# Kernel tuning notes

Measured on AMD Instinct MI355X. Metric: run time of the kernel, lower is better.

Reference implementation:

```python
import jax, jax.numpy as jnp
import numpy as np

B, C, E = 2, 1024, 1024
H = 16            # n_heads as declared (used as per-group feature dim due to module's reshape)
HD = E // H       # 64 — the axis actually batched over in attention


def setup_inputs() -> dict:
    key = jax.random.key(0)
    ks = jax.random.split(key, 5)
    scale = 0.02
    return {
        "x": jax.random.normal(ks[0], (B, C, E), dtype=jnp.float32),
        "W_q": jax.random.normal(ks[1], (E, E), dtype=jnp.float32) * scale,
        "W_k": jax.random.normal(ks[2], (E, E), dtype=jnp.float32) * scale,
        "W_v": jax.random.normal(ks[3], (E, E), dtype=jnp.float32) * scale,
        "W_o": jax.random.normal(ks[4], (E, E), dtype=jnp.float32) * scale,
    }


def reference(x, W_q, W_k, W_v, W_o):
    # nn.Linear: y = x @ W.T  (bias=False)
    def proj_split(W):
        y = jnp.einsum('bce,de->bcd', x, W)              # [B,C,E]
        # view(B, C, HD, H).transpose(1,2) -> [B, HD, C, H]  (faithful to source layout)
        return y.reshape(B, C, HD, H).transpose(0, 2, 1, 3)

    Q = proj_split(W_q)
    K = proj_split(W_k)
    V = proj_split(W_v)

    scale = 1.0 / jnp.sqrt(jnp.asarray(H, dtype=x.dtype))  # sqrt of last dim (= n_heads here)
    scores = jnp.einsum('bdqh,bdkh->bdqk', Q, K) * scale    # [B, HD, C, C]
    weights = jax.nn.softmax(scores, axis=-1)
    out = jnp.einsum('bdqk,bdkh->bdqh', weights, V)         # [B, HD, C, H]
    out = out.transpose(0, 2, 1, 3).reshape(B, C, E)        # [B, C, E]
    out = jnp.einsum('bce,de->bcd', out, W_o)
    return out  # dropout p=0.0 / eval mode: identity
```

## Files before the change

kernel.cpp:

```cpp
#include <hip/hip_runtime.h>
#include <stdint.h>
#include <math.h>


typedef __bf16   bf16x8 __attribute__((ext_vector_type(8)));
typedef float    f32x4  __attribute__((ext_vector_type(4)));

__device__ __forceinline__ unsigned short f2bf(float f) {
    unsigned int u = __float_as_uint(f);
    u += 0x7FFFu + ((u >> 16) & 1u);
    return (unsigned short)(u >> 16);
}
__device__ __forceinline__ float bflo(unsigned int u) { return __uint_as_float(u << 16); }
__device__ __forceinline__ float bfhi(unsigned int u) { return __uint_as_float(u & 0xFFFF0000u); }

__device__ __forceinline__ unsigned int pkbf(float lo, float hi) {
    const unsigned int ulo = __float_as_uint(lo) + 0x8000u;
    const unsigned int uhi = __float_as_uint(hi) + 0x8000u;
    return __builtin_amdgcn_perm(uhi, ulo, 0x07060302u);
}

__global__ __launch_bounds__(256) void cast_to_bf16(
    const float* __restrict__ x,
    const float* __restrict__ w0, const float* __restrict__ w1,
    const float* __restrict__ w2, const float* __restrict__ w3,
    unsigned short* __restrict__ xb,
    unsigned short* __restrict__ b0, unsigned short* __restrict__ b1,
    unsigned short* __restrict__ b2, unsigned short* __restrict__ b3)
{
    const int z = blockIdx.y;
    const float* src;
    unsigned short* dst;
    size_t off = 0;
    float sc = 1.f;
    if (z < 2)       { src = x;  dst = xb; off = (size_t)z << 20; }
    else if (z == 2) { src = w0; dst = b0; sc = 0.36067376022224085f; }
    else if (z == 3) { src = w1; dst = b1; }
    else if (z == 4) { src = w2; dst = b2; }
    else             { src = w3; dst = b3; }
    const size_t i = off + ((size_t)blockIdx.x * 256 + threadIdx.x) * 4;
    const float4 v = *(const float4*)(src + i);
    *(ushort4*)(dst + i) = make_ushort4(f2bf(v.x * sc), f2bf(v.y * sc),
                                        f2bf(v.z * sc), f2bf(v.w * sc));
}

__global__ __launch_bounds__(256) void gemm_bt_mfma(
    const unsigned short* __restrict__ A,
    const unsigned short* __restrict__ B0, const unsigned short* __restrict__ B1,
    const unsigned short* __restrict__ B2,
    void* __restrict__ C0, void* __restrict__ C1, void* __restrict__ C2,
    int M, int N, int K, int bf16out)
{
    const unsigned short* Bm = (blockIdx.z == 0) ? B0 : (blockIdx.z == 1) ? B1 : B2;
    void* Cm                 = (blockIdx.z == 0) ? C0 : (blockIdx.z == 1) ? C1 : C2;

    __shared__ __align__(16) unsigned short As[64 * 32];
    __shared__ __align__(16) unsigned short Bs[128 * 32];

    const int t    = threadIdx.x;
    const int lane = t & 63;
    const int w    = t >> 6;
    const int m0   = blockIdx.y * 64;
    const int n0   = blockIdx.x * 128;
    const int wm   = (w & 1) * 32;
    const int wn   = (w >> 1) * 64;

    const int r0 = t >> 2;
    const int c0 = (t & 3) * 8;
    const unsigned short* Apa = A  + (size_t)(m0 + r0) * K + c0;
    const unsigned short* Bpa = Bm + (size_t)(n0 + r0) * K + c0;
    const unsigned short* Bpb = Bm + (size_t)(n0 + r0 + 64) * K + c0;

    f32x4 acc[2][4];
#pragma unroll
    for (int i = 0; i < 2; ++i)
#pragma unroll
        for (int j = 0; j < 4; ++j) acc[i][j] = (f32x4){0.f, 0.f, 0.f, 0.f};

    const int fm = lane & 15;
    const int kg = lane >> 4;

    uint4 ra0 = *(const uint4*)(Apa);
    uint4 rb0 = *(const uint4*)(Bpa);
    uint4 rb1 = *(const uint4*)(Bpb);

    for (int k0 = 0; k0 < K; k0 += 32) {
        if (k0) __syncthreads();
        *(uint4*)&As[8 * t]        = ra0;
        *(uint4*)&Bs[8 * t]        = rb0;
        *(uint4*)&Bs[8 * t + 2048] = rb1;
        __syncthreads();

        if (k0 + 32 < K) {
            ra0 = *(const uint4*)(Apa + k0 + 32);
            rb0 = *(const uint4*)(Bpa + k0 + 32);
            rb1 = *(const uint4*)(Bpb + k0 + 32);
        }

        bf16x8 af[2], bfr[4];
#pragma unroll
        for (int im = 0; im < 2; ++im)
            af[im] = *(const bf16x8*)&As[(wm + im * 16 + fm) * 32 + kg * 8];
#pragma unroll
        for (int in = 0; in < 4; ++in)
            bfr[in] = *(const bf16x8*)&Bs[(wn + in * 16 + fm) * 32 + kg * 8];
#pragma unroll
        for (int im = 0; im < 2; ++im)
#pragma unroll
            for (int in = 0; in < 4; ++in)
                acc[im][in] = __builtin_amdgcn_mfma_f32_16x16x32_bf16(
                    af[im], bfr[in], acc[im][in], 0, 0, 0);
    }

#pragma unroll
    for (int im = 0; im < 2; ++im) {
#pragma unroll
        for (int in = 0; in < 4; ++in) {
            const int row = m0 + wm + im * 16 + kg * 4;
            const int col = n0 + wn + in * 16 + fm;
            if (bf16out) {
                unsigned short* cp = (unsigned short*)Cm;
#pragma unroll
                for (int r = 0; r < 4; ++r)
                    cp[(size_t)(row + r) * N + col] = f2bf(acc[im][in][r]);
            } else {
                float* cp = (float*)Cm;
#pragma unroll
                for (int r = 0; r < 4; ++r)
                    cp[(size_t)(row + r) * N + col] = acc[im][in][r];
            }
        }
    }
}

#define KSTR2 40
#define VSTR2 72
#define PSTR  80

__global__ __launch_bounds__(256) void attn_mfma(
    const unsigned short* __restrict__ Qb, const unsigned short* __restrict__ Kb,
    const unsigned short* __restrict__ Vb, unsigned short* __restrict__ Ob)
{
    __shared__ __align__(16) unsigned short Ks[64 * KSTR2];
    __shared__ __align__(16) unsigned short VsT[16 * VSTR2];
    __shared__ __align__(16) unsigned short Ps[128 * PSTR];
    __shared__ __align__(16) float Lsh[128];

    const int t    = threadIdx.x;
    const int lane = t & 63;
    const int wq   = t >> 6;
    const int fm   = lane & 15;
    const int kg   = lane >> 4;
    const int bh   = blockIdx.y;
    const size_t base = ((size_t)(bh >> 6) * 1024) * 1024 + (size_t)(bh & 63) * 16;
    const int q0 = blockIdx.x * 128;

    if (t < 128) {
        const int row = t >> 1, seg = t & 1;
        *(uint4*)&Ks[row * KSTR2 + 16 + seg * 8] = make_uint4(0, 0, 0, 0);
    }

    union { uint4 u; bf16x8 h; } zz; zz.u = make_uint4(0, 0, 0, 0);
    bf16x8 aq[2];
#pragma unroll
    for (int m = 0; m < 2; ++m) {
        if (kg < 2)
            aq[m] = *(const bf16x8*)(Qb + base +
                     (size_t)(q0 + wq * 32 + m * 16 + fm) * 1024 + kg * 8);
        else
            aq[m] = zz.h;
    }

    f32x4 oacc[2];
    float lp[2];
#pragma unroll
    for (int m = 0; m < 2; ++m) {
        oacc[m] = (f32x4){0.f, 0.f, 0.f, 0.f};
        lp[m] = 0.f;
    }

    for (int kt = 0; kt < 1024; kt += 64) {
        __syncthreads();
        if (t < 128) {
            const int row = t >> 1, seg = t & 1;
            *(uint4*)&Ks[row * KSTR2 + seg * 8] =
                *(const uint4*)(Kb + base + (size_t)(kt + row) * 1024 + seg * 8);
        } else {
            const int idx = t - 128;
            const int key = idx >> 1, half = idx & 1;
            uint4 v = *(const uint4*)(Vb + base + (size_t)(kt + key) * 1024 + half * 8);
            const unsigned short* pv = (const unsigned short*)&v;
#pragma unroll
            for (int d = 0; d < 8; ++d)
                VsT[(half * 8 + d) * VSTR2 + key] = pv[d];
        }
        __syncthreads();

        bf16x8 bk[4];
#pragma unroll
        for (int kn = 0; kn < 4; ++kn)
            bk[kn] = *(const bf16x8*)&Ks[(kn * 16 + fm) * KSTR2 + kg * 8];

#pragma unroll
        for (int kn = 0; kn < 4; ++kn) {
            f32x4 sm[2];
#pragma unroll
            for (int m = 0; m < 2; ++m)
                sm[m] = __builtin_amdgcn_mfma_f32_16x16x32_bf16(
                    bk[kn], aq[m], (f32x4){0.f, 0.f, 0.f, 0.f}, 0, 0, 0);
#pragma unroll
            for (int m = 0; m < 2; ++m) {
                const float p0 = __builtin_amdgcn_exp2f(sm[m][0]);
                const float p1 = __builtin_amdgcn_exp2f(sm[m][1]);
                const float p2 = __builtin_amdgcn_exp2f(sm[m][2]);
                const float p3 = __builtin_amdgcn_exp2f(sm[m][3]);
                lp[m] += (p0 + p1) + (p2 + p3);
                *(uint2*)&Ps[(wq * 32 + m * 16 + fm) * PSTR + kn * 16 + kg * 4] =
                    make_uint2(pkbf(p0, p1), pkbf(p2, p3));
            }
        }

        bf16x8 bv0 = *(const bf16x8*)&VsT[fm * VSTR2 + kg * 8];
        bf16x8 bv1 = *(const bf16x8*)&VsT[fm * VSTR2 + 32 + kg * 8];
#pragma unroll
        for (int m = 0; m < 2; ++m) {
            const int prow = wq * 32 + m * 16 + fm;
            bf16x8 ap0 = *(const bf16x8*)&Ps[prow * PSTR + kg * 8];
            bf16x8 ap1 = *(const bf16x8*)&Ps[prow * PSTR + 32 + kg * 8];
            oacc[m] = __builtin_amdgcn_mfma_f32_16x16x32_bf16(ap0, bv0, oacc[m], 0, 0, 0);
            oacc[m] = __builtin_amdgcn_mfma_f32_16x16x32_bf16(ap1, bv1, oacc[m], 0, 0, 0);
        }
    }

#pragma unroll
    for (int m = 0; m < 2; ++m) {
        float v = lp[m];
        v += __shfl_xor(v, 16, 64);
        v += __shfl_xor(v, 32, 64);
        if (kg == 0) Lsh[wq * 32 + m * 16 + fm] = v;
    }

#pragma unroll
    for (int m = 0; m < 2; ++m) {
        const float4 lr = *(const float4*)&Lsh[wq * 32 + m * 16 + kg * 4];
        const int qrow = q0 + wq * 32 + m * 16 + kg * 4;
        Ob[base + (size_t)(qrow + 0) * 1024 + fm] = f2bf(oacc[m][0] / lr.x);
        Ob[base + (size_t)(qrow + 1) * 1024 + fm] = f2bf(oacc[m][1] / lr.y);
        Ob[base + (size_t)(qrow + 2) * 1024 + fm] = f2bf(oacc[m][2] / lr.z);
        Ob[base + (size_t)(qrow + 3) * 1024 + fm] = f2bf(oacc[m][3] / lr.w);
    }
}

extern "C" void kernel_launch(void* const* d_in, const int* in_sizes, int n_in,
                              void* d_out, int out_size, void* d_ws, size_t ws_size,
                              hipStream_t stream) {
    const float* x  = (const float*)d_in[0];
    const float* Wq = (const float*)d_in[1];
    const float* Wk = (const float*)d_in[2];
    const float* Wv = (const float*)d_in[3];
    const float* Wo = (const float*)d_in[4];
    float* out = (float*)d_out;

    const int M = 2048, N = 1024, Kd = 1024;
    const size_t MEG = 1048576;
    unsigned short* ws = (unsigned short*)d_ws;
    unsigned short* xb  = ws;
    unsigned short* Wqb = ws + 2 * MEG;
    unsigned short* Wkb = ws + 3 * MEG;
    unsigned short* Wvb = ws + 4 * MEG;
    unsigned short* Wob = ws + 5 * MEG;
    unsigned short* Qb  = ws + 6 * MEG;
    unsigned short* Kb  = ws + 8 * MEG;
    unsigned short* Vb  = ws + 10 * MEG;
    unsigned short* Ob  = ws + 12 * MEG;

    dim3 gc(1024, 6, 1);
    cast_to_bf16<<<gc, 256, 0, stream>>>(x, Wq, Wk, Wv, Wo, xb, Wqb, Wkb, Wvb, Wob);

    dim3 g1(N / 128, M / 64, 3);
    gemm_bt_mfma<<<g1, 256, 0, stream>>>(xb, Wqb, Wkb, Wvb, Qb, Kb, Vb, M, N, Kd, 1);

    dim3 g2(8, 128, 1);
    attn_mfma<<<g2, 256, 0, stream>>>(Qb, Kb, Vb, Ob);

    dim3 g3(N / 128, M / 64, 1);
    gemm_bt_mfma<<<g3, 256, 0, stream>>>(Ob, Wob, Wob, Wob, out, out, out, M, N, Kd, 0);
}
```

Before: 150.3 us.

## Double-buffer K/V tiles in attention and widen GEMM K-step to 64

```diff
diff --git a/kernel.cpp b/kernel.cpp
--- a/kernel.cpp
+++ b/kernel.cpp
@@ -12,7 +12,6 @@
     return (unsigned short)(u >> 16);
 }
 __device__ __forceinline__ float bflo(unsigned int u) { return __uint_as_float(u << 16); }
-__device__ __forceinline__ float bfhi(unsigned int u) { return __uint_as_float(u & 0xFFFF0000u); }
 
 __device__ __forceinline__ unsigned int pkbf(float lo, float hi) {
     const unsigned int ulo = __float_as_uint(lo) + 0x8000u;
@@ -44,6 +43,8 @@
                                         f2bf(v.z * sc), f2bf(v.w * sc));
 }
 
+#define ASTR 72
+
 __global__ __launch_bounds__(256) void gemm_bt_mfma(
     const unsigned short* __restrict__ A,
     const unsigned short* __restrict__ B0, const unsigned short* __restrict__ B1,
@@ -54,8 +55,8 @@
     const unsigned short* Bm = (blockIdx.z == 0) ? B0 : (blockIdx.z == 1) ? B1 : B2;
     void* Cm                 = (blockIdx.z == 0) ? C0 : (blockIdx.z == 1) ? C1 : C2;
 
-    __shared__ __align__(16) unsigned short As[64 * 32];
-    __shared__ __align__(16) unsigned short Bs[128 * 32];
+    __shared__ __align__(16) unsigned short As[64 * ASTR];
+    __shared__ __align__(16) unsigned short Bs[128 * ASTR];
 
     const int t    = threadIdx.x;
     const int lane = t & 63;
@@ -65,11 +66,18 @@
     const int wm   = (w & 1) * 32;
     const int wn   = (w >> 1) * 64;
 
-    const int r0 = t >> 2;
-    const int c0 = (t & 3) * 8;
-    const unsigned short* Apa = A  + (size_t)(m0 + r0) * K + c0;
-    const unsigned short* Bpa = Bm + (size_t)(n0 + r0) * K + c0;
-    const unsigned short* Bpb = Bm + (size_t)(n0 + r0 + 64) * K + c0;
+    const int ar0 = t >> 3,           ac0 = (t & 7) * 8;
+    const int ar1 = (t + 256) >> 3,   ac1 = ac0;
+    const unsigned short* Ap0 = A + (size_t)(m0 + ar0) * K + ac0;
+    const unsigned short* Ap1 = A + (size_t)(m0 + ar1) * K + ac1;
+    const unsigned short* Bp[4];
+    int br[4], bc[4];
+#pragma unroll
+    for (int j = 0; j < 4; ++j) {
+        const int s = t + 256 * j;
+        br[j] = s >> 3; bc[j] = (s & 7) * 8;
+        Bp[j] = Bm + (size_t)(n0 + br[j]) * K + bc[j];
+    }
 
     f32x4 acc[2][4];
 #pragma unroll
@@ -80,36 +88,44 @@
     const int fm = lane & 15;
     const int kg = lane >> 4;
 
-    uint4 ra0 = *(const uint4*)(Apa);
-    uint4 rb0 = *(const uint4*)(Bpa);
-    uint4 rb1 = *(const uint4*)(Bpb);
-
-    for (int k0 = 0; k0 < K; k0 += 32) {
+    uint4 ra0 = *(const uint4*)(Ap0);
+    uint4 ra1 = *(const uint4*)(Ap1);
+    uint4 rb[4];
+#pragma unroll
+    for (int j = 0; j < 4; ++j) rb[j] = *(const uint4*)(Bp[j]);
+
+    for (int k0 = 0; k0 < K; k0 += 64) {
         if (k0) __syncthreads();
-        *(uint4*)&As[8 * t]        = ra0;
-        *(uint4*)&Bs[8 * t]        = rb0;
-        *(uint4*)&Bs[8 * t + 2048] = rb1;
+        *(uint4*)&As[ar0 * ASTR + ac0] = ra0;
+        *(uint4*)&As[ar1 * ASTR + ac1] = ra1;
+#pragma unroll
+        for (int j = 0; j < 4; ++j)
+            *(uint4*)&Bs[br[j] * ASTR + bc[j]] = rb[j];
         __syncthreads();
 
-        if (k0 + 32 < K) {
-            ra0 = *(const uint4*)(Apa + k0 + 32);
-            rb0 = *(const uint4*)(Bpa + k0 + 32);
-            rb1 = *(const uint4*)(Bpb + k0 + 32);
-        }
-
-        bf16x8 af[2], bfr[4];
-#pragma unroll
-        for (int im = 0; im < 2; ++im)
-            af[im] = *(const bf16x8*)&As[(wm + im * 16 + fm) * 32 + kg * 8];
-#pragma unroll
-        for (int in = 0; in < 4; ++in)
-            bfr[in] = *(const bf16x8*)&Bs[(wn + in * 16 + fm) * 32 + kg * 8];
-#pragma unroll
-        for (int im = 0; im < 2; ++im)
+        if (k0 + 64 < K) {
+            ra0 = *(const uint4*)(Ap0 + k0 + 64);
+            ra1 = *(const uint4*)(Ap1 + k0 + 64);
+#pragma unroll
+            for (int j = 0; j < 4; ++j) rb[j] = *(const uint4*)(Bp[j] + k0 + 64);
+        }
+
+#pragma unroll
+        for (int ks = 0; ks < 2; ++ks) {
+            bf16x8 af[2], bfr[4];
+#pragma unroll
+            for (int im = 0; im < 2; ++im)
+                af[im] = *(const bf16x8*)&As[(wm + im * 16 + fm) * ASTR + ks * 32 + kg * 8];
 #pragma unroll
             for (int in = 0; in < 4; ++in)
-                acc[im][in] = __builtin_amdgcn_mfma_f32_16x16x32_bf16(
-                    af[im], bfr[in], acc[im][in], 0, 0, 0);
+                bfr[in] = *(const bf16x8*)&Bs[(wn + in * 16 + fm) * ASTR + ks * 32 + kg * 8];
+#pragma unroll
+            for (int im = 0; im < 2; ++im)
+#pragma unroll
+                for (int in = 0; in < 4; ++in)
+                    acc[im][in] = __builtin_amdgcn_mfma_f32_16x16x32_bf16(
+                        af[im], bfr[in], acc[im][in], 0, 0, 0);
+        }
     }
 
 #pragma unroll
@@ -141,8 +157,8 @@
     const unsigned short* __restrict__ Qb, const unsigned short* __restrict__ Kb,
     const unsigned short* __restrict__ Vb, unsigned short* __restrict__ Ob)
 {
-    __shared__ __align__(16) unsigned short Ks[64 * KSTR2];
-    __shared__ __align__(16) unsigned short VsT[16 * VSTR2];
+    __shared__ __align__(16) unsigned short Ks[2][64 * KSTR2];
+    __shared__ __align__(16) unsigned short VsT[2][16 * VSTR2];
     __shared__ __align__(16) unsigned short Ps[128 * PSTR];
     __shared__ __align__(16) float Lsh[128];
 
@@ -155,9 +171,12 @@
     const size_t base = ((size_t)(bh >> 6) * 1024) * 1024 + (size_t)(bh & 63) * 16;
     const int q0 = blockIdx.x * 128;
 
+    const int krow = t >> 1,        kseg = t & 1;
+    const int vkey = (t - 128) >> 1, vhalf = (t - 128) & 1;
+
     if (t < 128) {
-        const int row = t >> 1, seg = t & 1;
-        *(uint4*)&Ks[row * KSTR2 + 16 + seg * 8] = make_uint4(0, 0, 0, 0);
+        *(uint4*)&Ks[0][krow * KSTR2 + 16 + kseg * 8] = make_uint4(0, 0, 0, 0);
+        *(uint4*)&Ks[1][krow * KSTR2 + 16 + kseg * 8] = make_uint4(0, 0, 0, 0);
     }
 
     union { uint4 u; bf16x8 h; } zz; zz.u = make_uint4(0, 0, 0, 0);
@@ -179,27 +198,37 @@
         lp[m] = 0.f;
     }
 
-    for (int kt = 0; kt < 1024; kt += 64) {
-        __syncthreads();
-        if (t < 128) {
-            const int row = t >> 1, seg = t & 1;
-            *(uint4*)&Ks[row * KSTR2 + seg * 8] =
-                *(const uint4*)(Kb + base + (size_t)(kt + row) * 1024 + seg * 8);
-        } else {
-            const int idx = t - 128;
-            const int key = idx >> 1, half = idx & 1;
-            uint4 v = *(const uint4*)(Vb + base + (size_t)(kt + key) * 1024 + half * 8);
-            const unsigned short* pv = (const unsigned short*)&v;
-#pragma unroll
-            for (int d = 0; d < 8; ++d)
-                VsT[(half * 8 + d) * VSTR2 + key] = pv[d];
-        }
-        __syncthreads();
+    uint4 rkv;
+    if (t < 128)
+        rkv = *(const uint4*)(Kb + base + (size_t)krow * 1024 + kseg * 8);
+    else
+        rkv = *(const uint4*)(Vb + base + (size_t)vkey * 1024 + vhalf * 8);
+
+    if (t < 128) {
+        *(uint4*)&Ks[0][krow * KSTR2 + kseg * 8] = rkv;
+    } else {
+        const unsigned short* pv = (const unsigned short*)&rkv;
+#pragma unroll
+        for (int d = 0; d < 8; ++d)
+            VsT[0][(vhalf * 8 + d) * VSTR2 + vkey] = pv[d];
+    }
+    __syncthreads();
+
+    for (int it = 0; it < 16; ++it) {
+        const int cur = it & 1;
+
+        if (it < 15) {
+            const int kt = (it + 1) * 64;
+            if (t < 128)
+                rkv = *(const uint4*)(Kb + base + (size_t)(kt + krow) * 1024 + kseg * 8);
+            else
+                rkv = *(const uint4*)(Vb + base + (size_t)(kt + vkey) * 1024 + vhalf * 8);
+        }
 
         bf16x8 bk[4];
 #pragma unroll
         for (int kn = 0; kn < 4; ++kn)
-            bk[kn] = *(const bf16x8*)&Ks[(kn * 16 + fm) * KSTR2 + kg * 8];
+            bk[kn] = *(const bf16x8*)&Ks[cur][(kn * 16 + fm) * KSTR2 + kg * 8];
 
 #pragma unroll
         for (int kn = 0; kn < 4; ++kn) {
@@ -220,8 +249,8 @@
             }
         }
 
-        bf16x8 bv0 = *(const bf16x8*)&VsT[fm * VSTR2 + kg * 8];
-        bf16x8 bv1 = *(const bf16x8*)&VsT[fm * VSTR2 + 32 + kg * 8];
+        bf16x8 bv0 = *(const bf16x8*)&VsT[cur][fm * VSTR2 + kg * 8];
+        bf16x8 bv1 = *(const bf16x8*)&VsT[cur][fm * VSTR2 + 32 + kg * 8];
 #pragma unroll
         for (int m = 0; m < 2; ++m) {
             const int prow = wq * 32 + m * 16 + fm;
@@ -230,6 +259,18 @@
             oacc[m] = __builtin_amdgcn_mfma_f32_16x16x32_bf16(ap0, bv0, oacc[m], 0, 0, 0);
             oacc[m] = __builtin_amdgcn_mfma_f32_16x16x32_bf16(ap1, bv1, oacc[m], 0, 0, 0);
         }
+
+        if (it < 15) {
+            if (t < 128) {
+                *(uint4*)&Ks[cur ^ 1][krow * KSTR2 + kseg * 8] = rkv;
+            } else {
+                const unsigned short* pv = (const unsigned short*)&rkv;
+#pragma unroll
+                for (int d = 0; d < 8; ++d)
+                    VsT[cur ^ 1][(vhalf * 8 + d) * VSTR2 + vkey] = pv[d];
+            }
+        }
+        __syncthreads();
     }
 
 #pragma unroll
```

Result: slower. 200.0 us (+33.1%).
